# Kernel optimization log

Measured on AMD Instinct MI355X. Metric: run time of the kernel, lower is better.

Reference implementation:

```python
import jax, jax.numpy as jnp
import numpy as np

N = 100000
E = 600000
D = 164
H = 2
DK = D // H
EDGE_DIM = 16
TIME_DIM = 8
STEP = 30000  # CFG.msg_chunk_edges


def setup_inputs() -> dict:
    key = jax.random.key(0)
    ks = jax.random.split(key, 14)
    q = jax.random.normal(ks[0], (N, D), dtype=jnp.float32)
    k = jax.random.normal(ks[1], (N, D), dtype=jnp.float32)
    v = jax.random.normal(ks[2], (N, D), dtype=jnp.float32)
    edge_index = jax.random.randint(ks[3], (2, E), 0, N, dtype=jnp.int32)
    edge_attr = jax.random.normal(ks[4], (E, EDGE_DIM), dtype=jnp.float32)
    edge_time = jax.random.uniform(ks[5], (E,), dtype=jnp.float32)
    # time_pe: Linear(1, time_dim)
    Wt = jax.random.normal(ks[6], (TIME_DIM, 1), dtype=jnp.float32) * 0.5
    bt = jax.random.normal(ks[7], (TIME_DIM,), dtype=jnp.float32) * 0.1
    # rel_film MLP: Linear(24, 82) -> ReLU -> Linear(82, 328)
    in_dim = EDGE_DIM + TIME_DIM
    W1 = jax.random.normal(ks[8], (D // 2, in_dim), dtype=jnp.float32) * (1.0 / np.sqrt(in_dim))
    b1 = jax.random.normal(ks[9], (D // 2,), dtype=jnp.float32) * 0.05
    W2 = jax.random.normal(ks[10], (2 * D, D // 2), dtype=jnp.float32) * (1.0 / np.sqrt(D // 2))
    b2 = jax.random.normal(ks[11], (2 * D,), dtype=jnp.float32) * 0.05
    rel_bias = jax.random.normal(ks[12], (H,), dtype=jnp.float32) * 0.02
    return {"q": q, "k": k, "v": v, "edge_index": edge_index,
            "edge_attr": edge_attr, "edge_time": edge_time,
            "Wt": Wt, "bt": bt, "W1": W1, "b1": b1, "W2": W2, "b2": b2,
            "rel_bias": rel_bias}


def reference(q, k, v, edge_index, edge_attr, edge_time, Wt, bt, W1, b1, W2, b2, rel_bias):
    n = q.shape[0]
    C = E // STEP  # number of edge chunks; softmax is per-chunk (dim=0 within chunk)
    src = edge_index[0].reshape(C, STEP)
    dst = edge_index[1].reshape(C, STEP)
    Q = q.reshape(n, H, DK)
    K = k.reshape(n, H, DK)
    V = v.reshape(n, H, DK)
    qh = Q[dst]  # [C, STEP, H, DK]
    kh = K[src]
    vh = V[src]
    # FiLM modulation from edge features + time positional encoding
    t_pe = edge_time.reshape(C, STEP, 1) * Wt[:, 0] + bt  # [C, STEP, TIME_DIM]
    feat = jnp.concatenate([edge_attr.reshape(C, STEP, EDGE_DIM), t_pe], axis=-1)
    hmid = jax.nn.relu(jnp.einsum('cef,of->ceo', feat, W1) + b1)
    gb = jnp.einsum('ceo,go->ceg', hmid, W2) + b2  # [C, STEP, 2*D]
    gamma, beta = jnp.split(gb, 2, axis=-1)
    gamma = jnp.tanh(gamma).reshape(C, STEP, H, DK)
    beta = jnp.tanh(beta).reshape(C, STEP, H, DK)
    vh = vh * (1.0 + gamma) + beta
    # attention score + per-chunk softmax over edges (matches torch dim=0 softmax per chunk)
    score = jnp.sum(qh * kh, axis=-1) / np.sqrt(DK).astype(np.float32) + rel_bias  # [C, STEP, H]
    att = jax.nn.softmax(score, axis=1)
    m = (att[..., None] * vh).reshape(C * STEP, D)
    out = jnp.zeros((n, D), dtype=q.dtype).at[dst.reshape(-1)].add(m)
    return out  # dropout is identity in eval mode
```

## Files before the change

### kernel.cpp

```cpp
#include <hip/hip_runtime.h>

#define NN 100000
#define EE 600000
#define DD 164
#define HH 2
#define DKK 82
#define EDIM 16
#define TDIM 8
#define STEP 30000
#define NC 20
#define FEAT 24
#define HID 82
#define NG 41
#define KP 96
#define MP 336
#define NBLK ((EE + 255) / 256)

typedef __attribute__((ext_vector_type(8))) short short8;
typedef __attribute__((ext_vector_type(4))) float floatx4;

__device__ __forceinline__ float fast_tanh(float x) {
    float e = __expf(2.0f * x);
    return 1.0f - 2.0f * __builtin_amdgcn_rcpf(e + 1.0f);
}

__device__ __forceinline__ short f2bf(float f) {
    union { float f; unsigned u; } x; x.f = f;
    unsigned r = x.u + 0x7fffu + ((x.u >> 16) & 1u);
    return (short)(r >> 16);
}


__global__ void __launch_bounds__(256) prep_w2_kernel(
    const float* __restrict__ W2, const float* __restrict__ b2,
    short* __restrict__ W2p, float* __restrict__ b2p)
{
    int idx = blockIdx.x * 256 + threadIdx.x;
    if (idx < MP * KP) {
        int m = idx / KP, kk = idx - m * KP;
        float val = 0.f;
        if (m < 2 * DD && kk < HID) {
            int dth = m >> 1, p = m & 1;
            val = W2[(size_t)(dth + p * DD) * HID + kk];
        }
        W2p[idx] = f2bf(val);
    }
    if (idx < MP) {
        float bv = 0.f;
        if (idx < 2 * DD) { int dth = idx >> 1, p = idx & 1; bv = b2[dth + p * DD]; }
        b2p[idx] = bv;
    }
}


__global__ void __launch_bounds__(256) zero2_kernel(int* __restrict__ a, int* __restrict__ b, int n) {
    int i = blockIdx.x * 256 + threadIdx.x;
    if (i < n) { a[i] = 0; b[i] = 0; }
}

__global__ void __launch_bounds__(256) count_kernel(const int* __restrict__ ei, int* __restrict__ deg) {
    int e = blockIdx.x * 256 + threadIdx.x;
    if (e < EE) atomicAdd(&deg[ei[EE + e]], 1);
}

__global__ void __launch_bounds__(256) scan_kernel(const int* __restrict__ deg, int* __restrict__ off) {
    const int CH = (NN + 255) / 256;
    int t = threadIdx.x;
    int beg = t * CH, end = min(beg + CH, NN);
    int s = 0;
    for (int i = beg; i < end; ++i) s += deg[i];
    __shared__ int sums[256];
    sums[t] = s;
    __syncthreads();
    for (int d = 1; d < 256; d <<= 1) {
        int val = (t >= d) ? sums[t - d] : 0;
        __syncthreads();
        sums[t] += val;
        __syncthreads();
    }
    int run = (t == 0) ? 0 : sums[t - 1];
    for (int i = beg; i < end; ++i) { off[i] = run; run += deg[i]; }
    if (t == 255) off[NN] = run;
}

__global__ void __launch_bounds__(256) fill_kernel(const int* __restrict__ ei,
                                                   const int* __restrict__ off,
                                                   int* __restrict__ cnt,
                                                   int* __restrict__ elist) {
    int e = blockIdx.x * 256 + threadIdx.x;
    if (e >= EE) return;
    int d = ei[EE + e];
    int p = atomicAdd(&cnt[d], 1);
    elist[off[d] + p] = e;
}


__global__ void __launch_bounds__(256) score_coop_kernel(
    const float* __restrict__ q, const float* __restrict__ k,
    const int* __restrict__ ei, const float* __restrict__ rel_bias,
    const int* __restrict__ elist, float* __restrict__ escore)
{
    const int tid = threadIdx.x;
    const int grp = tid >> 4;
    const int gl  = tid & 15;
    int i = blockIdx.x * 16 + grp;
    if (i >= EE) return;
    int e = elist[i];
    int sn = ei[e];
    int dn = ei[EE + e];
    const float4* qr = (const float4*)(q + (size_t)dn * DD);
    const float4* kr = (const float4*)(k + (size_t)sn * DD);
    float s0 = 0.f, s1 = 0.f;
    #pragma unroll
    for (int jj = 0; jj < 3; ++jj) {
        int idx = gl + 16 * jj;
        if (idx < 41) {
            float4 a = qr[idx], b = kr[idx];
            float lo = a.x * b.x + a.y * b.y;
            float hi = a.z * b.z + a.w * b.w;
            s0 += (idx < 20 ? hi : 0.f) + (idx <= 20 ? lo : 0.f);
            s1 += (idx > 20 ? lo : 0.f) + (idx >= 20 ? hi : 0.f);
        }
    }
    #pragma unroll
    for (int m = 1; m < 16; m <<= 1) {
        s0 += __shfl_xor(s0, m, 64);
        s1 += __shfl_xor(s1, m, 64);
    }
    if (gl == 0) {
        const float inv_sqrt = 0.11043152607484654f;
        escore[2 * e]     = __expf(s0 * inv_sqrt + rel_bias[0]);
        escore[2 * e + 1] = __expf(s1 * inv_sqrt + rel_bias[1]);
    }
}

__global__ void __launch_bounds__(256) score_kernel(
    const float* __restrict__ q, const float* __restrict__ k,
    const int* __restrict__ ei, const float* __restrict__ rel_bias,
    float* __restrict__ escore)
{
    int e = blockIdx.x * 256 + threadIdx.x;
    if (e >= EE) return;
    int s = ei[e];
    int d = ei[EE + e];
    const float4* qr = (const float4*)(q + (size_t)d * DD);
    const float4* kr = (const float4*)(k + (size_t)s * DD);
    float s0 = 0.f, s1 = 0.f;
    #pragma unroll 4
    for (int i = 0; i < 20; ++i) {
        float4 a = qr[i], b = kr[i];
        s0 += a.x * b.x; s0 += a.y * b.y; s0 += a.z * b.z; s0 += a.w * b.w;
    }
    {
        float4 a = qr[20], b = kr[20];
        s0 += a.x * b.x + a.y * b.y;
        s1 += a.z * b.z + a.w * b.w;
    }
    #pragma unroll 4
    for (int i = 21; i < 41; ++i) {
        float4 a = qr[i], b = kr[i];
        s1 += a.x * b.x; s1 += a.y * b.y; s1 += a.z * b.z; s1 += a.w * b.w;
    }
    const float inv_sqrt = 0.11043152607484654f;
    escore[2 * e]     = __expf(s0 * inv_sqrt + rel_bias[0]);
    escore[2 * e + 1] = __expf(s1 * inv_sqrt + rel_bias[1]);
}

__global__ void __launch_bounds__(256) chunkinv_kernel(
    const float* __restrict__ escore, float* __restrict__ invsum)
{
    int c = blockIdx.x, h = blockIdx.y;
    const float* base = escore + (size_t)c * STEP * 2 + h;
    float acc = 0.f;
    for (int i = threadIdx.x; i < STEP; i += 256) acc += base[2 * i];
    __shared__ float red[256];
    red[threadIdx.x] = acc;
    __syncthreads();
    for (int s2 = 128; s2 > 0; s2 >>= 1) {
        if (threadIdx.x < s2) red[threadIdx.x] += red[threadIdx.x + s2];
        __syncthreads();
    }
    if (threadIdx.x == 0) invsum[c * 2 + h] = 1.0f / red[0];
}

__global__ void __launch_bounds__(256) zero_kernel(float4* __restrict__ p, int n4) {
    int i = blockIdx.x * 256 + threadIdx.x;
    if (i < n4) p[i] = make_float4(0.f, 0.f, 0.f, 0.f);
}


__global__ void __launch_bounds__(256) main_mfma_kernel(
    const float* __restrict__ v, const int* __restrict__ ei,
    const float* __restrict__ edge_attr, const float* __restrict__ edge_time,
    const float* __restrict__ Wt, const float* __restrict__ bt,
    const float* __restrict__ W1, const float* __restrict__ b1,
    const short* __restrict__ W2p, const float* __restrict__ b2p,
    const float* __restrict__ escore, const float* __restrict__ invsum,
    const int* __restrict__ off, const int* __restrict__ elist,
    float* __restrict__ out)
{
    __shared__ short hmid_lds[256 * KP];
    __shared__ float res_lds[256 * 8];
    __shared__ int   sdst[256];
    __shared__ int   ssrc[256];
    __shared__ float satt[512];

    const int tid = threadIdx.x;
    const int gid = blockIdx.x * 256 + tid;
    const bool valid = gid < EE;
    const int gi = valid ? gid : (EE - 1);
    const int e = elist[gi];
    const int s = ei[e];
    const int d = ei[EE + e];
    sdst[tid] = valid ? d : -1;
    ssrc[tid] = s;
    {
        unsigned c = (unsigned)e / STEP;
        satt[2 * tid]     = escore[2 * e]     * invsum[2 * c];
        satt[2 * tid + 1] = escore[2 * e + 1] * invsum[2 * c + 1];
    }

    float feat[FEAT];
    const float4* ea4 = (const float4*)(edge_attr + (size_t)e * EDIM);
    #pragma unroll
    for (int i = 0; i < 4; ++i) {
        float4 a = ea4[i];
        feat[4 * i + 0] = a.x; feat[4 * i + 1] = a.y;
        feat[4 * i + 2] = a.z; feat[4 * i + 3] = a.w;
    }
    float t = edge_time[e];
    #pragma unroll
    for (int j = 0; j < TDIM; ++j) feat[EDIM + j] = t * Wt[j] + bt[j];

    #pragma unroll 1
    for (int oc = 0; oc < KP / 8; ++oc) {
        union { short h[8]; int4 v4; } pk;
        #pragma unroll
        for (int j = 0; j < 8; ++j) {
            int o = oc * 8 + j;
            float acc = 0.f;
            if (o < HID) {
                acc = b1[o];
                #pragma unroll
                for (int f = 0; f < FEAT; ++f) acc = fmaf(feat[f], W1[o * FEAT + f], acc);
                acc = fmaxf(acc, 0.f);
            }
            pk.h[j] = f2bf(acc);
        }
        *(int4*)&hmid_lds[tid * KP + oc * 8] = pk.v4;
    }
    __syncthreads();

    const int lane = tid & 63;
    const int wavebase = tid & ~63;
    const int lrow = lane & 15;
    const int quad = lane >> 4;

    short8 bfrag[4][3];
    #pragma unroll
    for (int nt = 0; nt < 4; ++nt)
        #pragma unroll
        for (int ks = 0; ks < 3; ++ks)
            bfrag[nt][ks] = *(const short8*)&hmid_lds[(wavebase + nt * 16 + lrow) * KP + ks * 32 + quad * 8];

    bool leader = valid && (tid == 0 || sdst[tid - 1] != d);
    int seglen = 0;
    bool interior = false;
    float* orow = nullptr;
    if (leader) {
        while (tid + seglen < 256 && sdst[tid + seglen] == d) ++seglen;
        int bs = blockIdx.x * 256;
        interior = (off[d] >= bs) && (off[d + 1] <= bs + 256);
        orow = out + (size_t)d * DD;
    }

    #pragma unroll 1
    for (int mt = 0; mt < 21; ++mt) {
        short8 afrag[3];
        #pragma unroll
        for (int ks = 0; ks < 3; ++ks)
            afrag[ks] = *(const short8*)&W2p[(mt * 16 + lrow) * KP + ks * 32 + quad * 8];

        floatx4 acc[4];
        #pragma unroll
        for (int nt = 0; nt < 4; ++nt) acc[nt] = (floatx4)(0.f);
        #pragma unroll
        for (int ks = 0; ks < 3; ++ks)
            #pragma unroll
            for (int nt = 0; nt < 4; ++nt)
                acc[nt] = __builtin_amdgcn_mfma_f32_16x16x32_bf16(afrag[ks], bfrag[nt][ks], acc[nt], 0, 0, 0);

        float4 bias = *(const float4*)&b2p[mt * 16 + quad * 4];
        int d0 = mt * 8 + quad * 2;

        #pragma unroll
        for (int nt = 0; nt < 4; ++nt) {
            int e_loc = wavebase + nt * 16 + lrow;
            float r0 = 0.f, r1 = 0.f;
            if (d0 < DD) {
                float g0  = fast_tanh(acc[nt][0] + bias.x);
                float be0 = fast_tanh(acc[nt][1] + bias.y);
                float g1  = fast_tanh(acc[nt][2] + bias.z);
                float be1 = fast_tanh(acc[nt][3] + bias.w);
                int s_e = ssrc[e_loc];
                const float* vp = v + (size_t)s_e * DD + d0;
                float v0 = vp[0], v1 = vp[1];
                float a0 = satt[2 * e_loc + (d0 >= DKK ? 1 : 0)];
                float a1 = satt[2 * e_loc + (d0 + 1 >= DKK ? 1 : 0)];
                r0 = a0 * (v0 * (1.f + g0) + be0);
                r1 = a1 * (v1 * (1.f + g1) + be1);
            }
            res_lds[e_loc * 8 + quad * 2]     = r0;
            res_lds[e_loc * 8 + quad * 2 + 1] = r1;
        }
        __syncthreads();

        if (leader) {
            float4 s0 = make_float4(0.f, 0.f, 0.f, 0.f);
            float4 s1 = make_float4(0.f, 0.f, 0.f, 0.f);
            for (int t2 = 0; t2 < seglen; ++t2) {
                const float4* rp = (const float4*)&res_lds[(tid + t2) * 8];
                float4 a = rp[0], b = rp[1];
                s0.x += a.x; s0.y += a.y; s0.z += a.z; s0.w += a.w;
                s1.x += b.x; s1.y += b.y; s1.z += b.z; s1.w += b.w;
            }
            int D0 = mt * 8;
            if (interior) {
                *(float4*)(orow + D0) = s0;
                if (D0 + 4 < DD) *(float4*)(orow + D0 + 4) = s1;
            } else {
                unsafeAtomicAdd(orow + D0 + 0, s0.x);
                unsafeAtomicAdd(orow + D0 + 1, s0.y);
                unsafeAtomicAdd(orow + D0 + 2, s0.z);
                unsafeAtomicAdd(orow + D0 + 3, s0.w);
                if (D0 + 4 < DD) {
                    unsafeAtomicAdd(orow + D0 + 4, s1.x);
                    unsafeAtomicAdd(orow + D0 + 5, s1.y);
                    unsafeAtomicAdd(orow + D0 + 6, s1.z);
                    unsafeAtomicAdd(orow + D0 + 7, s1.w);
                }
            }
        }
        __syncthreads();
    }
}


__global__ void __launch_bounds__(256) main_atomic_kernel(
    const float* __restrict__ v, const int* __restrict__ ei,
    const float* __restrict__ edge_attr, const float* __restrict__ edge_time,
    const float* __restrict__ Wt, const float* __restrict__ bt,
    const float* __restrict__ W1, const float* __restrict__ b1,
    const float* __restrict__ W2, const float* __restrict__ b2,
    const float* __restrict__ escore, const float* __restrict__ invsum,
    float* __restrict__ out)
{
    int e = blockIdx.x * 256 + threadIdx.x;
    if (e >= EE) return;
    int s = ei[e];
    int d = ei[EE + e];
    float feat[FEAT];
    const float4* ea4 = (const float4*)(edge_attr + (size_t)e * EDIM);
    #pragma unroll
    for (int i = 0; i < 4; ++i) {
        float4 a = ea4[i];
        feat[4 * i + 0] = a.x; feat[4 * i + 1] = a.y;
        feat[4 * i + 2] = a.z; feat[4 * i + 3] = a.w;
    }
    float t = edge_time[e];
    #pragma unroll
    for (int j = 0; j < TDIM; ++j) feat[EDIM + j] = t * Wt[j] + bt[j];
    float hmid[HID];
    #pragma unroll
    for (int o = 0; o < HID; ++o) {
        float acc = b1[o];
        #pragma unroll
        for (int f = 0; f < FEAT; ++f) acc = fmaf(feat[f], W1[o * FEAT + f], acc);
        hmid[o] = fmaxf(acc, 0.f);
    }
    int c = e / STEP;
    float att0 = escore[2 * e]     * invsum[2 * c];
    float att1 = escore[2 * e + 1] * invsum[2 * c + 1];
    const float4* vrow4 = (const float4*)(v + (size_t)s * DD);
    float* orow = out + (size_t)d * DD;
    #pragma unroll 1
    for (int j = 0; j < NG; ++j) {
        float4 vv = vrow4[j];
        float vvals[4] = {vv.x, vv.y, vv.z, vv.w};
        float res[4];
        #pragma unroll
        for (int u = 0; u < 4; ++u) {
            int dd = 4 * j + u;
            float ga = b2[dd];
            float bb = b2[dd + DD];
            #pragma unroll
            for (int o = 0; o < HID; ++o) {
                ga = fmaf(hmid[o], W2[dd * HID + o], ga);
                bb = fmaf(hmid[o], W2[(dd + DD) * HID + o], bb);
            }
            float gamma = fast_tanh(ga);
            float beta  = fast_tanh(bb);
            float vh = vvals[u] * (1.f + gamma) + beta;
            res[u] = ((dd < DKK) ? att0 : att1) * vh;
        }
        unsafeAtomicAdd(orow + 4 * j + 0, res[0]);
        unsafeAtomicAdd(orow + 4 * j + 1, res[1]);
        unsafeAtomicAdd(orow + 4 * j + 2, res[2]);
        unsafeAtomicAdd(orow + 4 * j + 3, res[3]);
    }
}


extern "C" void kernel_launch(void* const* d_in, const int* in_sizes, int n_in,
                              void* d_out, int out_size, void* d_ws, size_t ws_size,
                              hipStream_t stream) {
    const float* q   = (const float*)d_in[0];
    const float* k   = (const float*)d_in[1];
    const float* v   = (const float*)d_in[2];
    const int*   ei  = (const int*)d_in[3];
    const float* ea  = (const float*)d_in[4];
    const float* et  = (const float*)d_in[5];
    const float* Wt  = (const float*)d_in[6];
    const float* bt  = (const float*)d_in[7];
    const float* W1  = (const float*)d_in[8];
    const float* b1  = (const float*)d_in[9];
    const float* W2  = (const float*)d_in[10];
    const float* b2  = (const float*)d_in[11];
    const float* rb  = (const float*)d_in[12];
    float* out = (float*)d_out;

    short* W2p    = (short*)d_ws;
    float* b2p    = (float*)(W2p + MP * KP);
    float* escore = b2p + MP;
    float* invsum = escore + (size_t)2 * EE;
    int*   deg    = (int*)(invsum + 64);
    int*   off    = deg + NN;
    int*   cnt    = off + NN + 1;
    int*   elist  = cnt + NN;

    size_t need = (size_t)(MP * KP) * 2 + (MP + 2 * EE + 64) * 4 +
                  ((size_t)3 * NN + 1 + EE) * 4;

    int n4 = out_size / 4;
    zero_kernel<<<(n4 + 255) / 256, 256, 0, stream>>>((float4*)out, n4);

    if (ws_size >= need) {
        prep_w2_kernel<<<(MP * KP + 255) / 256, 256, 0, stream>>>(W2, b2, W2p, b2p);
        zero2_kernel<<<(NN + 255) / 256, 256, 0, stream>>>(deg, cnt, NN);
        count_kernel<<<NBLK, 256, 0, stream>>>(ei, deg);
        scan_kernel<<<1, 256, 0, stream>>>(deg, off);
        fill_kernel<<<NBLK, 256, 0, stream>>>(ei, off, cnt, elist);
        score_coop_kernel<<<(EE + 15) / 16, 256, 0, stream>>>(q, k, ei, rb, elist, escore);
        chunkinv_kernel<<<dim3(NC, HH), 256, 0, stream>>>(escore, invsum);
        main_mfma_kernel<<<NBLK, 256, 0, stream>>>(
            v, ei, ea, et, Wt, bt, W1, b1, W2p, b2p, escore, invsum, off, elist, out);
    } else {
        float* escore_f = (float*)d_ws;
        float* invsum_f = escore_f + (size_t)2 * EE;
        score_kernel<<<NBLK, 256, 0, stream>>>(q, k, ei, rb, escore_f);
        chunkinv_kernel<<<dim3(NC, HH), 256, 0, stream>>>(escore_f, invsum_f);
        main_atomic_kernel<<<NBLK, 256, 0, stream>>>(
            v, ei, ea, et, Wt, bt, W1, b1, W2, b2, escore_f, invsum_f, out);
    }
}
```

Baseline: 964.2 us.

## Split FiLM GEMM and destination-owned reduction through an fp16 gamma/beta buffer

```diff
diff --git a/kernel.cpp b/kernel.cpp
--- a/kernel.cpp
+++ b/kernel.cpp
@@ -30,6 +30,17 @@
     return (short)(r >> 16);
 }
 
+__device__ __forceinline__ unsigned pack_f16(float g, float b) {
+    union { _Float16 h[2]; unsigned u; } p;
+    p.h[0] = (_Float16)g; p.h[1] = (_Float16)b;
+    return p.u;
+}
+
+__device__ __forceinline__ float2 unpack_f16(unsigned x) {
+    union { unsigned u; _Float16 h[2]; } p; p.u = x;
+    return make_float2((float)p.h[0], (float)p.h[1]);
+}
+
 
 __global__ void __launch_bounds__(256) prep_w2_kernel(
     const float* __restrict__ W2, const float* __restrict__ b2,
@@ -86,12 +97,15 @@
 __global__ void __launch_bounds__(256) fill_kernel(const int* __restrict__ ei,
                                                    const int* __restrict__ off,
                                                    int* __restrict__ cnt,
-                                                   int* __restrict__ elist) {
+                                                   int* __restrict__ elist,
+                                                   int* __restrict__ srcp) {
     int e = blockIdx.x * 256 + threadIdx.x;
     if (e >= EE) return;
     int d = ei[EE + e];
     int p = atomicAdd(&cnt[d], 1);
-    elist[off[d] + p] = e;
+    int slot = off[d] + p;
+    elist[slot] = e;
+    if (srcp) srcp[slot] = ei[e];
 }
 
 
@@ -186,6 +200,156 @@
 __global__ void __launch_bounds__(256) zero_kernel(float4* __restrict__ p, int n4) {
     int i = blockIdx.x * 256 + threadIdx.x;
     if (i < n4) p[i] = make_float4(0.f, 0.f, 0.f, 0.f);
+}
+
+
+__global__ void __launch_bounds__(256) gemm_film_kernel(
+    const int* __restrict__ ei,
+    const float* __restrict__ edge_attr, const float* __restrict__ edge_time,
+    const float* __restrict__ Wt, const float* __restrict__ bt,
+    const float* __restrict__ W1, const float* __restrict__ b1,
+    const short* __restrict__ W2p, const float* __restrict__ b2p,
+    const float* __restrict__ escore, const float* __restrict__ invsum,
+    const int* __restrict__ elist,
+    unsigned* __restrict__ gbp, float* __restrict__ attp)
+{
+    __shared__ short hmid_lds[256 * KP];
+
+    const int tid = threadIdx.x;
+    const int bs  = blockIdx.x * 256;
+    const int gid = bs + tid;
+    const bool valid = gid < EE;
+    const int gi = valid ? gid : (EE - 1);
+    const int e = elist[gi];
+    if (valid) {
+        unsigned c = (unsigned)e / STEP;
+        attp[2 * gid]     = escore[2 * e]     * invsum[2 * c];
+        attp[2 * gid + 1] = escore[2 * e + 1] * invsum[2 * c + 1];
+    }
+
+    float feat[FEAT];
+    const float4* ea4 = (const float4*)(edge_attr + (size_t)e * EDIM);
+    #pragma unroll
+    for (int i = 0; i < 4; ++i) {
+        float4 a = ea4[i];
+        feat[4 * i + 0] = a.x; feat[4 * i + 1] = a.y;
+        feat[4 * i + 2] = a.z; feat[4 * i + 3] = a.w;
+    }
+    float t = edge_time[e];
+    #pragma unroll
+    for (int j = 0; j < TDIM; ++j) feat[EDIM + j] = t * Wt[j] + bt[j];
+
+    #pragma unroll 1
+    for (int oc = 0; oc < KP / 8; ++oc) {
+        union { short h[8]; int4 v4; } pk;
+        #pragma unroll
+        for (int j = 0; j < 8; ++j) {
+            int o = oc * 8 + j;
+            float acc = 0.f;
+            if (o < HID) {
+                acc = b1[o];
+                #pragma unroll
+                for (int f = 0; f < FEAT; ++f) acc = fmaf(feat[f], W1[o * FEAT + f], acc);
+                acc = fmaxf(acc, 0.f);
+            }
+            pk.h[j] = f2bf(acc);
+        }
+        *(int4*)&hmid_lds[tid * KP + oc * 8] = pk.v4;
+    }
+    __syncthreads();
+
+    const int lane = tid & 63;
+    const int wavebase = tid & ~63;
+    const int lrow = lane & 15;
+    const int quad = lane >> 4;
+
+    short8 bfrag[4][3];
+    #pragma unroll
+    for (int nt = 0; nt < 4; ++nt)
+        #pragma unroll
+        for (int ks = 0; ks < 3; ++ks)
+            bfrag[nt][ks] = *(const short8*)&hmid_lds[(wavebase + nt * 16 + lrow) * KP + ks * 32 + quad * 8];
+
+    #pragma unroll 1
+    for (int mt = 0; mt < 21; ++mt) {
+        short8 afrag[3];
+        #pragma unroll
+        for (int ks = 0; ks < 3; ++ks)
+            afrag[ks] = *(const short8*)&W2p[(mt * 16 + lrow) * KP + ks * 32 + quad * 8];
+
+        floatx4 acc[4];
+        #pragma unroll
+        for (int nt = 0; nt < 4; ++nt) acc[nt] = (floatx4)(0.f);
+        #pragma unroll
+        for (int ks = 0; ks < 3; ++ks)
+            #pragma unroll
+            for (int nt = 0; nt < 4; ++nt)
+                acc[nt] = __builtin_amdgcn_mfma_f32_16x16x32_bf16(afrag[ks], bfrag[nt][ks], acc[nt], 0, 0, 0);
+
+        float4 bias = *(const float4*)&b2p[mt * 16 + quad * 4];
+        int d0 = mt * 8 + quad * 2;
+
+        if (d0 < DD) {
+            #pragma unroll
+            for (int nt = 0; nt < 4; ++nt) {
+                int e_loc = wavebase + nt * 16 + lrow;
+                int slot = bs + e_loc;
+                if (slot < EE) {
+                    float g0  = fast_tanh(acc[nt][0] + bias.x);
+                    float be0 = fast_tanh(acc[nt][1] + bias.y);
+                    float g1  = fast_tanh(acc[nt][2] + bias.z);
+                    float be1 = fast_tanh(acc[nt][3] + bias.w);
+                    uint2 pk;
+                    pk.x = pack_f16(g0, be0);
+                    pk.y = pack_f16(g1, be1);
+                    *(uint2*)&gbp[(size_t)slot * DD + d0] = pk;
+                }
+            }
+        }
+    }
+}
+
+
+__global__ void __launch_bounds__(256) reduce_kernel(
+    const float* __restrict__ v, const int* __restrict__ off,
+    const int* __restrict__ srcp, const float* __restrict__ attp,
+    const unsigned* __restrict__ gbp, float* __restrict__ out)
+{
+    int gw   = (blockIdx.x * 256 + threadIdx.x) >> 6;
+    int lane = threadIdx.x & 63;
+    if (gw >= NN) return;
+    int beg = off[gw], end = off[gw + 1];
+
+    const int d1 = lane + 64;
+    const int d2 = lane + 128;
+    const bool has2 = (d2 < DD);
+    float acc0 = 0.f, acc1 = 0.f, acc2 = 0.f;
+
+    for (int sl = beg; sl < end; ++sl) {
+        int src = srcp[sl];
+        float t0 = attp[2 * sl];
+        float t1 = attp[2 * sl + 1];
+        const float*    vr = v   + (size_t)src * DD;
+        const unsigned* gr = gbp + (size_t)sl  * DD;
+
+        unsigned g0 = gr[lane], g1 = gr[d1];
+        float    v0 = vr[lane], v1 = vr[d1];
+        float2 gb0 = unpack_f16(g0);
+        float2 gb1 = unpack_f16(g1);
+        acc0 += t0 * (v0 * (1.f + gb0.x) + gb0.y);
+        float ts = (d1 < DKK) ? t0 : t1;
+        acc1 += ts * (v1 * (1.f + gb1.x) + gb1.y);
+        if (has2) {
+            unsigned g2 = gr[d2];
+            float    v2 = vr[d2];
+            float2 gb2 = unpack_f16(g2);
+            acc2 += t1 * (v2 * (1.f + gb2.x) + gb2.y);
+        }
+    }
+    float* orow = out + (size_t)gw * DD;
+    orow[lane] = acc0;
+    orow[d1]   = acc1;
+    if (has2) orow[d2] = acc2;
 }
 
 
@@ -429,27 +593,56 @@
     const float* rb  = (const float*)d_in[12];
     float* out = (float*)d_out;
 
-    short* W2p    = (short*)d_ws;
-    float* b2p    = (float*)(W2p + MP * KP);
-    float* escore = b2p + MP;
-    float* invsum = escore + (size_t)2 * EE;
-    int*   deg    = (int*)(invsum + 64);
-    int*   off    = deg + NN;
-    int*   cnt    = off + NN + 1;
-    int*   elist  = cnt + NN;
-
-    size_t need = (size_t)(MP * KP) * 2 + (MP + 2 * EE + 64) * 4 +
-                  ((size_t)3 * NN + 1 + EE) * 4;
-
-    int n4 = out_size / 4;
-    zero_kernel<<<(n4 + 255) / 256, 256, 0, stream>>>((float4*)out, n4);
-
-    if (ws_size >= need) {
+    size_t need2 = (size_t)(MP * KP) * 2 + (MP + 2 * EE + 64) * 4 +
+                   ((size_t)3 * NN + 1 + EE) * 4;
+    size_t need3 = (size_t)EE * DD * 4
+                 + (size_t)(MP * KP) * 2 + (MP + 2 * EE + 64) * 4
+                 + ((size_t)3 * NN + 1) * 4
+                 + (size_t)EE * 4
+                 + (size_t)EE * 4
+                 + (size_t)2 * EE * 4;
+
+    if (ws_size >= need3) {
+        unsigned* gbp  = (unsigned*)d_ws;
+        short* W2p     = (short*)(gbp + (size_t)EE * DD);
+        float* b2p     = (float*)(W2p + MP * KP);
+        float* escore  = b2p + MP;
+        float* invsum  = escore + (size_t)2 * EE;
+        int*   deg     = (int*)(invsum + 64);
+        int*   off     = deg + NN;
+        int*   cnt     = off + NN + 1;
+        int*   elist   = cnt + NN;
+        int*   srcp    = elist + EE;
+        float* attp    = (float*)(srcp + EE);
+
         prep_w2_kernel<<<(MP * KP + 255) / 256, 256, 0, stream>>>(W2, b2, W2p, b2p);
         zero2_kernel<<<(NN + 255) / 256, 256, 0, stream>>>(deg, cnt, NN);
         count_kernel<<<NBLK, 256, 0, stream>>>(ei, deg);
         scan_kernel<<<1, 256, 0, stream>>>(deg, off);
-        fill_kernel<<<NBLK, 256, 0, stream>>>(ei, off, cnt, elist);
+        fill_kernel<<<NBLK, 256, 0, stream>>>(ei, off, cnt, elist, srcp);
+        score_coop_kernel<<<(EE + 15) / 16, 256, 0, stream>>>(q, k, ei, rb, elist, escore);
+        chunkinv_kernel<<<dim3(NC, HH), 256, 0, stream>>>(escore, invsum);
+        gemm_film_kernel<<<NBLK, 256, 0, stream>>>(
+            ei, ea, et, Wt, bt, W1, b1, W2p, b2p, escore, invsum, elist, gbp, attp);
+        reduce_kernel<<<(NN * 64 + 255) / 256, 256, 0, stream>>>(
+            v, off, srcp, attp, gbp, out);
+    } else if (ws_size >= need2) {
+        short* W2p    = (short*)d_ws;
+        float* b2p    = (float*)(W2p + MP * KP);
+        float* escore = b2p + MP;
+        float* invsum = escore + (size_t)2 * EE;
+        int*   deg    = (int*)(invsum + 64);
+        int*   off    = deg + NN;
+        int*   cnt    = off + NN + 1;
+        int*   elist  = cnt + NN;
+
+        int n4 = out_size / 4;
+        zero_kernel<<<(n4 + 255) / 256, 256, 0, stream>>>((float4*)out, n4);
+        prep_w2_kernel<<<(MP * KP + 255) / 256, 256, 0, stream>>>(W2, b2, W2p, b2p);
+        zero2_kernel<<<(NN + 255) / 256, 256, 0, stream>>>(deg, cnt, NN);
+        count_kernel<<<NBLK, 256, 0, stream>>>(ei, deg);
+        scan_kernel<<<1, 256, 0, stream>>>(deg, off);
+        fill_kernel<<<NBLK, 256, 0, stream>>>(ei, off, cnt, elist, (int*)nullptr);
         score_coop_kernel<<<(EE + 15) / 16, 256, 0, stream>>>(q, k, ei, rb, elist, escore);
         chunkinv_kernel<<<dim3(NC, HH), 256, 0, stream>>>(escore, invsum);
         main_mfma_kernel<<<NBLK, 256, 0, stream>>>(
@@ -457,6 +650,8 @@
     } else {
         float* escore_f = (float*)d_ws;
         float* invsum_f = escore_f + (size_t)2 * EE;
+        int n4 = out_size / 4;
+        zero_kernel<<<(n4 + 255) / 256, 256, 0, stream>>>((float4*)out, n4);
         score_kernel<<<NBLK, 256, 0, stream>>>(q, k, ei, rb, escore_f);
         chunkinv_kernel<<<dim3(NC, HH), 256, 0, stream>>>(escore_f, invsum_f);
         main_atomic_kernel<<<NBLK, 256, 0, stream>>>(
```

Measured after the change: 967.2 us. Within noise of the previous version (+0.3%).
